# Kernel tuning notes

Hardware: AMD Instinct MI355X
Metric: run time of the kernel (lower is better)

Reference implementation:

```python
import jax, jax.numpy as jnp
import numpy as np

N, F_IN, HID, EMB, HEADS, E = 20000, 256, 256, 128, 8, 160000
NEG_SLOPE = 0.2


def setup_inputs() -> dict:
    key = jax.random.key(0)
    ks = jax.random.split(key, 16)
    s = lambda fan: 1.0 / np.sqrt(fan)
    inp = {
        "x": jax.random.normal(ks[0], (N, F_IN), jnp.float32),
        "edge_index": jax.random.randint(ks[1], (2, E), 0, N, jnp.int64),
        "W1": jax.random.normal(ks[2], (F_IN, HID), jnp.float32) * s(F_IN),
        "b1": jnp.zeros((HID,), jnp.float32),
        "W2": jax.random.normal(ks[3], (HID, HID), jnp.float32) * s(HID),
        "b2": jnp.zeros((HID,), jnp.float32),
        "W3": jax.random.normal(ks[4], (HID, EMB), jnp.float32) * s(HID),
        "b3": jnp.zeros((EMB,), jnp.float32),
        "Wg": jax.random.normal(ks[5], (EMB, HEADS * EMB), jnp.float32) * s(EMB),
        "att_src": jax.random.normal(ks[6], (HEADS, EMB), jnp.float32) * s(EMB),
        "att_dst": jax.random.normal(ks[7], (HEADS, EMB), jnp.float32) * s(EMB),
        "bg": jnp.zeros((HEADS * EMB,), jnp.float32),
        "Wh1": jax.random.normal(ks[8], (HEADS * EMB, HID), jnp.float32) * s(HEADS * EMB),
        "bh1": jnp.zeros((HID,), jnp.float32),
        "Wh2": jax.random.normal(ks[9], (HID, 1), jnp.float32) * s(HID),
        "bh2": jnp.zeros((1,), jnp.float32),
    }
    return inp


def _gcn(x, W, b, src, dst, dinv):
    h = x @ W                                   # [N, out]
    msg = h[src] * (dinv[src] * dinv[dst])[:, None]  # gather + edge scale
    return jax.ops.segment_sum(msg, dst, N) + b


def _gat(x, Wg, att_src, att_dst, bg, src, dst):
    h = (x @ Wg).reshape(N, HEADS, EMB)          # [N, H, C]
    a_s = jnp.einsum('nhc,hc->nh', h, att_src)   # [N, H]
    a_d = jnp.einsum('nhc,hc->nh', h, att_dst)
    e = jax.nn.leaky_relu(a_s[src] + a_d[dst], NEG_SLOPE)  # [Etot, H]
    m = jax.ops.segment_max(e, dst, N)           # per-dst softmax max
    ex = jnp.exp(e - m[dst])
    denom = jax.ops.segment_sum(ex, dst, N)
    alpha = ex / denom[dst]                      # [Etot, H]
    out = jax.ops.segment_sum(h[src] * alpha[:, :, None], dst, N)
    return out.reshape(N, HEADS * EMB) + bg


def reference(x, edge_index, W1, b1, W2, b2, W3, b3, Wg, att_src, att_dst, bg, Wh1, bh1, Wh2, bh2):
    loops = jnp.arange(N, dtype=edge_index.dtype)
    src = jnp.concatenate([edge_index[0], loops])
    dst = jnp.concatenate([edge_index[1], loops])
    deg = jax.ops.segment_sum(jnp.ones_like(dst, dtype=x.dtype), dst, N)
    dinv = jax.lax.rsqrt(jnp.maximum(deg, 1.0))  # deg >= 1 due to self-loops

    h = jax.nn.relu(_gcn(x, W1, b1, src, dst, dinv))
    h = jax.nn.relu(_gcn(h, W2, b2, src, dst, dinv))
    h = jax.nn.relu(_gcn(h, W3, b3, src, dst, dinv))
    h = _gat(h, Wg, att_src, att_dst, bg, src, dst)
    z = jax.nn.relu(h @ Wh1 + bh1)
    logits = (z @ Wh2 + bh2).squeeze(-1)         # [N]
    w = jax.nn.sigmoid(logits)
    return jax.nn.softmax(w, axis=0)
```

## Files before the change

kernel.cpp:

```cpp
#include <hip/hip_runtime.h>
#include <math.h>

#define NN 20000
#define HEADS 8
#define M_PAD 20096

typedef _Float16 f16;
typedef f16 f16x2  __attribute__((ext_vector_type(2)));
typedef f16 f16x4v __attribute__((ext_vector_type(4)));
typedef f16 f16x8v __attribute__((ext_vector_type(8)));
typedef float f32x4 __attribute__((ext_vector_type(4)));

__device__ __forceinline__ float lrelu(float x){ return x > 0.f ? x : 0.2f*x; }

__global__ __launch_bounds__(256) void init_k(int* __restrict__ zbase, int zn,
        const float* __restrict__ W1, const float* __restrict__ W2, const float* __restrict__ W3,
        const float* __restrict__ Wg, const float* __restrict__ att_src, const float* __restrict__ att_dst,
        f16* __restrict__ wt1, f16* __restrict__ wt2, f16* __restrict__ wt3,
        f16* __restrict__ wasT)
{
    int t = blockIdx.x*256 + threadIdx.x;
    if (t < zn){ zbase[t] = 0; return; }
    t -= zn;
    if (t < 65536){ int k = t >> 8, n = t & 255; wt1[n*256 + k] = (f16)W1[t]; return; }
    t -= 65536;
    if (t < 65536){ int k = t >> 8, n = t & 255; wt2[n*256 + k] = (f16)W2[t]; return; }
    t -= 65536;
    if (t < 32768){ int k = t >> 7, n = t & 127; wt3[n*256 + k] = (f16)W3[t]; return; }
    t -= 32768;
    if (t < 8192){
        int r = t >> 7, k = t & 127;
        float s = 0.f;
        if (r < 16){
            const float* att = (r < 8) ? att_src : att_dst;
            int h = r & 7;
            const float* wg = Wg + (size_t)k*1024 + h*128;
            const float* at = att + h*128;
            for (int c = 0; c < 128; ++c) s = fmaf(wg[c], at[c], s);
        }
        wasT[r*128 + k] = (f16)s;
    }
}

__global__ __launch_bounds__(256) void wc_k(const float* __restrict__ Wg, const float* __restrict__ Wh1,
        const float* __restrict__ bg, const float* __restrict__ bh1,
        f16* __restrict__ wc_t, float* __restrict__ biasc)
{
    __shared__ float col[1024];
    __shared__ float red[256];
    const int j = blockIdx.x, t = threadIdx.x;
    float bsum = 0.f;
    #pragma unroll
    for (int i = 0; i < 4; ++i){
        int kk = i*256 + t;
        float v = Wh1[(size_t)kk*256 + j];
        col[kk] = v;
        bsum = fmaf(bg[kk], v, bsum);
    }
    red[t] = bsum; __syncthreads();
    for (int off = 128; off; off >>= 1){
        if (t < off) red[t] += red[t+off];
        __syncthreads();
    }
    if (!t) biasc[j] = red[0] + bh1[j];
    #pragma unroll
    for (int i = 0; i < 4; ++i){
        int k = i*256 + t;
        int h = k >> 7, kk = k & 127;
        const float* wg = Wg + (size_t)kk*1024 + h*128;
        const float* cl = col + h*128;
        float s = 0.f;
        for (int c = 0; c < 128; c += 4){
            float4 wv = *(const float4*)(wg + c);
            s = fmaf(wv.x, cl[c],   s);
            s = fmaf(wv.y, cl[c+1], s);
            s = fmaf(wv.z, cl[c+2], s);
            s = fmaf(wv.w, cl[c+3], s);
        }
        wc_t[(size_t)j*1024 + k] = (f16)s;
    }
}

__global__ __launch_bounds__(256) void hist_k(const int* __restrict__ dst, int* __restrict__ cnt, int E){
    int i = blockIdx.x*256 + threadIdx.x;
    if (i < E) atomicAdd(&cnt[dst[i]], 1);
}
__global__ __launch_bounds__(1024) void scan_k(const int* __restrict__ cnt, int* __restrict__ row_off,
                                               float* __restrict__ dinv){
    __shared__ int tot[1024];
    int t = threadIdx.x;
    const int CH = 20;
    int base = t*CH;
    int loc[CH]; int s = 0;
    #pragma unroll
    for (int i = 0; i < CH; ++i){
        int v = (base+i < NN) ? cnt[base+i] : 0;
        loc[i] = s; s += v;
    }
    tot[t] = s; __syncthreads();
    for (int off = 1; off < 1024; off <<= 1){
        int v = (t >= off) ? tot[t-off] : 0;
        __syncthreads();
        tot[t] += v;
        __syncthreads();
    }
    int pre = (t == 0) ? 0 : tot[t-1];
    #pragma unroll
    for (int i = 0; i < CH; ++i)
        if (base+i < NN){
            row_off[base+i] = pre + loc[i];
            dinv[base+i] = rsqrtf((float)cnt[base+i] + 1.f);
        }
    if (t == 1023) row_off[NN] = tot[1023];
}
__global__ __launch_bounds__(256) void scatter_k(const int* __restrict__ src, const int* __restrict__ dst,
        const int* __restrict__ row_off, int* __restrict__ cursor, int* __restrict__ src_sorted, int E){
    int i = blockIdx.x*256 + threadIdx.x;
    if (i >= E) return;
    int d = dst[i];
    int pos = row_off[d] + atomicAdd(&cursor[d], 1);
    src_sorted[pos] = src[i];
}

template<int EPI, int BN, bool A_F32, bool RELU, bool HAS_BIAS, int MINW>
__global__ __launch_bounds__(256, MINW) void gemm_f16_k(
        const void* __restrict__ Av, const f16* __restrict__ Bt,
        const float* __restrict__ bias, void* __restrict__ C,
        float* __restrict__ as_out, float* __restrict__ ad_out,
        const float* __restrict__ Wh2, float* __restrict__ logit,
        int M, int N, int K)
{
    constexpr int WN = BN/2;
    constexpr int NJ = WN/16;
    __shared__ __align__(16) f16 As[128*64];
    __shared__ __align__(16) f16 Bs[BN*64];
    const int tid  = threadIdx.x;
    const int lane = tid & 63;
    const int wave = tid >> 6;
    const int wm = (wave >> 1) * 64, wn = (wave & 1) * WN;
    const int l15 = lane & 15, quad = lane >> 4;
    const int m0 = blockIdx.y * 128, n0 = blockIdx.x * BN;

    const int rs = tid >> 3;
    const int ce = (tid & 7) * 8;
    const int swst = ((rs & 7) << 3);
    const int swrd = ((l15 & 7) << 3);
    const f16*  Ah = (const f16*)Av;
    const float* Af = (const float*)Av;

    f32x4 acc[4][NJ] = {};
    for (int k0 = 0; k0 < K; k0 += 64){
        #pragma unroll
        for (int pp = 0; pp < 4; ++pp){
            int lr = rs + pp*32;
            int grow = m0 + lr;
            if (A_F32){
                f16x8v hv = {};
                if (grow < M){
                    float4 p = *(const float4*)(Af + (size_t)grow*K + k0 + ce);
                    float4 q = *(const float4*)(Af + (size_t)grow*K + k0 + ce + 4);
                    hv[0]=(f16)p.x; hv[1]=(f16)p.y; hv[2]=(f16)p.z; hv[3]=(f16)p.w;
                    hv[4]=(f16)q.x; hv[5]=(f16)q.y; hv[6]=(f16)q.z; hv[7]=(f16)q.w;
                }
                *(f16x8v*)&As[lr*64 + (ce ^ swst)] = hv;
            } else {
                *(uint4*)&As[lr*64 + (ce ^ swst)] = *(const uint4*)(Ah + (size_t)grow*K + k0 + ce);
            }
        }
        #pragma unroll
        for (int pp = 0; pp < BN/32; ++pp){
            int lr = rs + pp*32;
            *(uint4*)&Bs[lr*64 + (ce ^ swst)] = *(const uint4*)(Bt + (size_t)(n0 + lr)*K + k0 + ce);
        }
        __syncthreads();
        #pragma unroll
        for (int ks = 0; ks < 2; ++ks){
            f16x8v af[4], bf[NJ];
            const int rc = (ks*32 + quad*8) ^ swrd;
            #pragma unroll
            for (int i = 0; i < 4; ++i)
                af[i] = *(const f16x8v*)&As[(wm + i*16 + l15)*64 + rc];
            #pragma unroll
            for (int j = 0; j < NJ; ++j)
                bf[j] = *(const f16x8v*)&Bs[(wn + j*16 + l15)*64 + rc];
            #pragma unroll
            for (int i = 0; i < 4; ++i)
                #pragma unroll
                for (int j = 0; j < NJ; ++j)
                    acc[i][j] = __builtin_amdgcn_mfma_f32_16x16x32_f16(af[i], bf[j], acc[i][j], 0, 0, 0);
        }
        __syncthreads();
    }

    if (EPI == 2){
        float b4[NJ], w4[NJ];
        #pragma unroll
        for (int j = 0; j < NJ; ++j){
            int cg = n0 + wn + j*16 + l15;
            b4[j] = bias[cg]; w4[j] = Wh2[cg];
        }
        #pragma unroll
        for (int i = 0; i < 4; ++i)
            #pragma unroll
            for (int r = 0; r < 4; ++r){
                float ps = 0.f;
                #pragma unroll
                for (int j = 0; j < NJ; ++j){
                    float v = fmaxf(acc[i][j][r] + b4[j], 0.f);
                    ps = fmaf(v, w4[j], ps);
                }
                ps += __shfl_xor(ps, 1, 64); ps += __shfl_xor(ps, 2, 64);
                ps += __shfl_xor(ps, 4, 64); ps += __shfl_xor(ps, 8, 64);
                if (l15 == 0){
                    int row = m0 + wm + i*16 + quad*4 + r;
                    if (row < M) unsafeAtomicAdd(&logit[row], ps);
                }
            }
        return;
    }

    if (EPI == 3){
        #pragma unroll
        for (int i = 0; i < 4; ++i){
            int rb = m0 + wm + i*16 + quad*4;
            #pragma unroll
            for (int j = 0; j < NJ; ++j){
                int col = n0 + wn + j*16 + l15;
                if (col >= 16) continue;
                #pragma unroll
                for (int r = 0; r < 4; ++r){
                    int row = rb + r;
                    if (row >= M) continue;
                    float v = acc[i][j][r];
                    if (col < 8) as_out[row*8 + col] = v;
                    else         ad_out[row*8 + col - 8] = v;
                }
            }
        }
        return;
    }

    #pragma unroll
    for (int i = 0; i < 4; ++i){
        int rb = m0 + wm + i*16 + quad*4;
        #pragma unroll
        for (int j = 0; j < NJ; ++j){
            int col = n0 + wn + j*16 + l15;
            float bv = HAS_BIAS ? bias[col] : 0.f;
            #pragma unroll
            for (int r = 0; r < 4; ++r){
                int row = rb + r;
                if (row >= M) continue;
                float v = acc[i][j][r] + bv;
                if (RELU) v = fmaxf(v, 0.f);
                ((f16*)C)[(size_t)row*N + col] = (f16)v;
            }
        }
    }
}

template<int F>
__global__ __launch_bounds__(256) void gcn_agg_f16_k(const f16* __restrict__ h, const int* __restrict__ row_off,
        const int* __restrict__ srcs, const float* __restrict__ dinv, const float* __restrict__ bias,
        f16* __restrict__ out)
{
    int wv = (blockIdx.x*256 + threadIdx.x) >> 6;
    int lane = threadIdx.x & 63;
    if (wv >= NN) return;
    float di = dinv[wv];
    int p = row_off[wv], r1 = row_off[wv+1];
    if (F == 256){
        f16x4v v = *(const f16x4v*)(h + (size_t)wv*256 + lane*4);
        float c = di*di;
        float a0 = (float)v[0]*c, a1 = (float)v[1]*c, a2 = (float)v[2]*c, a3 = (float)v[3]*c;
        for (; p+4 <= r1; p += 4){
            int s0 = srcs[p], s1 = srcs[p+1], s2 = srcs[p+2], s3 = srcs[p+3];
            float c0 = dinv[s0]*di, c1 = dinv[s1]*di, c2 = dinv[s2]*di, c3 = dinv[s3]*di;
            f16x4v u0 = *(const f16x4v*)(h + (size_t)s0*256 + lane*4);
            f16x4v u1 = *(const f16x4v*)(h + (size_t)s1*256 + lane*4);
            f16x4v u2 = *(const f16x4v*)(h + (size_t)s2*256 + lane*4);
            f16x4v u3 = *(const f16x4v*)(h + (size_t)s3*256 + lane*4);
            a0 = fmaf((float)u3[0], c3, fmaf((float)u2[0], c2, fmaf((float)u1[0], c1, fmaf((float)u0[0], c0, a0))));
            a1 = fmaf((float)u3[1], c3, fmaf((float)u2[1], c2, fmaf((float)u1[1], c1, fmaf((float)u0[1], c0, a1))));
            a2 = fmaf((float)u3[2], c3, fmaf((float)u2[2], c2, fmaf((float)u1[2], c1, fmaf((float)u0[2], c0, a2))));
            a3 = fmaf((float)u3[3], c3, fmaf((float)u2[3], c2, fmaf((float)u1[3], c1, fmaf((float)u0[3], c0, a3))));
        }
        for (; p < r1; ++p){
            int s0 = srcs[p];
            float c0 = dinv[s0]*di;
            f16x4v u0 = *(const f16x4v*)(h + (size_t)s0*256 + lane*4);
            a0 = fmaf((float)u0[0], c0, a0); a1 = fmaf((float)u0[1], c0, a1);
            a2 = fmaf((float)u0[2], c0, a2); a3 = fmaf((float)u0[3], c0, a3);
        }
        float4 bv = *(const float4*)(bias + lane*4);
        f16x4v o;
        o[0] = (f16)fmaxf(a0 + bv.x, 0.f); o[1] = (f16)fmaxf(a1 + bv.y, 0.f);
        o[2] = (f16)fmaxf(a2 + bv.z, 0.f); o[3] = (f16)fmaxf(a3 + bv.w, 0.f);
        *(f16x4v*)(out + (size_t)wv*256 + lane*4) = o;
    } else {
        f16x2 v = *(const f16x2*)(h + (size_t)wv*128 + lane*2);
        float c = di*di;
        float a0 = (float)v[0]*c, a1 = (float)v[1]*c;
        for (; p+4 <= r1; p += 4){
            int s0 = srcs[p], s1 = srcs[p+1], s2 = srcs[p+2], s3 = srcs[p+3];
            float c0 = dinv[s0]*di, c1 = dinv[s1]*di, c2 = dinv[s2]*di, c3 = dinv[s3]*di;
            f16x2 u0 = *(const f16x2*)(h + (size_t)s0*128 + lane*2);
            f16x2 u1 = *(const f16x2*)(h + (size_t)s1*128 + lane*2);
            f16x2 u2 = *(const f16x2*)(h + (size_t)s2*128 + lane*2);
            f16x2 u3 = *(const f16x2*)(h + (size_t)s3*128 + lane*2);
            a0 = fmaf((float)u3[0], c3, fmaf((float)u2[0], c2, fmaf((float)u1[0], c1, fmaf((float)u0[0], c0, a0))));
            a1 = fmaf((float)u3[1], c3, fmaf((float)u2[1], c2, fmaf((float)u1[1], c1, fmaf((float)u0[1], c0, a1))));
        }
        for (; p < r1; ++p){
            int s0 = srcs[p];
            float c0 = dinv[s0]*di;
            f16x2 u0 = *(const f16x2*)(h + (size_t)s0*128 + lane*2);
            a0 = fmaf((float)u0[0], c0, a0); a1 = fmaf((float)u0[1], c0, a1);
        }
        float2 bv = *(const float2*)(bias + lane*2);
        f16x2 o;
        o[0] = (f16)fmaxf(a0 + bv.x, 0.f); o[1] = (f16)fmaxf(a1 + bv.y, 0.f);
        *(f16x2*)(out + (size_t)wv*128 + lane*2) = o;
    }
}

__global__ __launch_bounds__(256) void gat_soft_k(const int* __restrict__ row_off, const int* __restrict__ srcs,
        const float* __restrict__ a_s, const float* __restrict__ a_d,
        float* __restrict__ ex_sorted, float* __restrict__ alpha_self, float* __restrict__ inv_den)
{
    int t = blockIdx.x*256 + threadIdx.x;
    if (t >= NN*HEADS) return;
    int d = t >> 3, h = t & 7;
    float ad = a_d[t];
    float eself = lrelu(a_s[t] + ad);
    float m = eself;
    int r0 = row_off[d], r1 = row_off[d+1];
    for (int p = r0; p < r1; ++p){
        int s = srcs[p];
        m = fmaxf(m, lrelu(a_s[s*HEADS + h] + ad));
    }
    float den = __expf(eself - m);
    for (int p = r0; p < r1; ++p){
        int s = srcs[p];
        float x = __expf(lrelu(a_s[s*HEADS + h] + ad) - m);
        ex_sorted[(size_t)p*HEADS + h] = x;
        den += x;
    }
    float id = 1.f / den;
    alpha_self[t] = __expf(eself - m) * id;
    inv_den[t]    = id;
}

__global__ __launch_bounds__(256) void agg_k(const f16* __restrict__ fG, const int* __restrict__ row_off,
        const int* __restrict__ srcs, const float* __restrict__ exs, const float* __restrict__ aself,
        const float* __restrict__ idn, f16* __restrict__ agg)
{
    int wv = (blockIdx.x*256 + threadIdx.x) >> 6;
    int lane = threadIdx.x & 63;
    if (wv >= NN) return;
    f16x2 v = *(const f16x2*)(fG + (size_t)wv*128 + lane*2);
    float v0 = (float)v[0], v1 = (float)v[1];
    float id[8], acc0[8], acc1[8];
    #pragma unroll
    for (int h = 0; h < 8; ++h){
        float as = aself[wv*8 + h];
        acc0[h] = v0*as; acc1[h] = v1*as;
        id[h] = idn[wv*8 + h];
    }
    int p = row_off[wv], r1 = row_off[wv+1];
    for (; p+2 <= r1; p += 2){
        int s0 = srcs[p], s1 = srcs[p+1];
        f16x2 u0 = *(const f16x2*)(fG + (size_t)s0*128 + lane*2);
        f16x2 u1 = *(const f16x2*)(fG + (size_t)s1*128 + lane*2);
        float4 ea = *(const float4*)(exs + (size_t)p*8);
        float4 eb = *(const float4*)(exs + (size_t)p*8 + 4);
        float4 fa = *(const float4*)(exs + (size_t)(p+1)*8);
        float4 fb = *(const float4*)(exs + (size_t)(p+1)*8 + 4);
        float u00=(float)u0[0], u01=(float)u0[1], u10=(float)u1[0], u11=(float)u1[1];
        float e0[8] = {ea.x,ea.y,ea.z,ea.w,eb.x,eb.y,eb.z,eb.w};
        float e1[8] = {fa.x,fa.y,fa.z,fa.w,fb.x,fb.y,fb.z,fb.w};
        #pragma unroll
        for (int h = 0; h < 8; ++h){
            float al0 = e0[h]*id[h], al1 = e1[h]*id[h];
            acc0[h] = fmaf(u10, al1, fmaf(u00, al0, acc0[h]));
            acc1[h] = fmaf(u11, al1, fmaf(u01, al0, acc1[h]));
        }
    }
    for (; p < r1; ++p){
        int s0 = srcs[p];
        f16x2 u0 = *(const f16x2*)(fG + (size_t)s0*128 + lane*2);
        float4 ea = *(const float4*)(exs + (size_t)p*8);
        float4 eb = *(const float4*)(exs + (size_t)p*8 + 4);
        float u00=(float)u0[0], u01=(float)u0[1];
        float e0[8] = {ea.x,ea.y,ea.z,ea.w,eb.x,eb.y,eb.z,eb.w};
        #pragma unroll
        for (int h = 0; h < 8; ++h){
            float al0 = e0[h]*id[h];
            acc0[h] = fmaf(u00, al0, acc0[h]);
            acc1[h] = fmaf(u01, al0, acc1[h]);
        }
    }
    #pragma unroll
    for (int h = 0; h < 8; ++h){
        f16x2 o; o[0] = (f16)acc0[h]; o[1] = (f16)acc1[h];
        *(f16x2*)(agg + (size_t)wv*1024 + h*128 + lane*2) = o;
    }
}

__global__ __launch_bounds__(256) void head_sum_k(const float* __restrict__ logit, const float* __restrict__ bh2,
                                                  float* __restrict__ w, float* __restrict__ red){
    __shared__ float sm[256];
    int i = blockIdx.x*256 + threadIdx.x;
    float v = 0.f;
    if (i < NN){
        float s = 1.f / (1.f + expf(-(logit[i] + bh2[0])));
        w[i] = s;
        v = expf(s);
    }
    sm[threadIdx.x] = v; __syncthreads();
    for (int off = 128; off; off >>= 1){
        if (threadIdx.x < off) sm[threadIdx.x] += sm[threadIdx.x+off];
        __syncthreads();
    }
    if (!threadIdx.x) unsafeAtomicAdd(&red[0], sm[0]);
}
__global__ __launch_bounds__(256) void final_k(const float* __restrict__ w, const float* __restrict__ red,
                                               float* __restrict__ out){
    int i = blockIdx.x*256 + threadIdx.x;
    if (i >= NN) return;
    out[i] = expf(w[i]) / red[0];
}

extern "C" void kernel_launch(void* const* d_in, const int* in_sizes, int n_in,
                              void* d_out, int out_size, void* d_ws, size_t ws_size,
                              hipStream_t stream) {
    const float* x   = (const float*)d_in[0];
    const int*   ei  = (const int*)  d_in[1];
    const float* W1  = (const float*)d_in[2];
    const float* b1  = (const float*)d_in[3];
    const float* W2  = (const float*)d_in[4];
    const float* b2  = (const float*)d_in[5];
    const float* W3  = (const float*)d_in[6];
    const float* b3  = (const float*)d_in[7];
    const float* Wg  = (const float*)d_in[8];
    const float* att_src = (const float*)d_in[9];
    const float* att_dst = (const float*)d_in[10];
    const float* bg  = (const float*)d_in[11];
    const float* Wh1 = (const float*)d_in[12];
    const float* bh1 = (const float*)d_in[13];
    const float* Wh2 = (const float*)d_in[14];
    const float* bh2 = (const float*)d_in[15];
    float* out = (float*)d_out;

    const int E = in_sizes[1] / 2;
    const int* src = ei;
    const int* dst = ei + E;

    float* ws = (float*)d_ws;
    size_t o = 0;
    auto alloc = [&](size_t nfloats){ float* p = ws + o; o += (nfloats + 3) & ~(size_t)3; return p; };
    int* cnt    = (int*)alloc(NN);
    int* cursor = (int*)alloc(NN);
    float* logit= alloc(NN);
    float* red  = alloc(8);
    const int ZERO_N = 3*NN + 8;

    f16* wt1   = (f16*)alloc(65536/2);
    f16* wt2   = (f16*)alloc(65536/2);
    f16* wt3   = (f16*)alloc(32768/2);
    f16* wc_t  = (f16*)alloc(262144/2);
    f16* wasT  = (f16*)alloc(8192/2);
    float* biasc = alloc(256);
    f16* fH    = (f16*)alloc((size_t)M_PAD*256/2);
    f16* fG    = (f16*)alloc((size_t)M_PAD*256/2);
    f16* agg   = (f16*)alloc((size_t)M_PAD*1024/2);
    float* dinv = alloc(NN);
    float* a_s  = alloc((size_t)NN*HEADS);
    float* a_d  = alloc((size_t)NN*HEADS);
    float* aself= alloc((size_t)NN*HEADS);
    float* idn  = alloc((size_t)NN*HEADS);
    float* exs  = alloc((size_t)E*HEADS);
    float* wsig = alloc(NN);
    int* row_off= (int*)alloc(NN+1);
    int* src_srt= (int*)alloc(E);

    const int nb  = (NN + 255)/256;
    const int eb  = (E + 255)/256;
    const int nwb = (NN + 3)/4;
    const dim3 blk(256);
    const int MT = M_PAD/128;

    const int INIT_T = ZERO_N + 65536*2 + 32768 + 8192;
    init_k<<<(INIT_T + 255)/256, blk, 0, stream>>>(cnt, ZERO_N, W1, W2, W3, Wg, att_src, att_dst,
                                                   wt1, wt2, wt3, wasT);
    wc_k<<<256, blk, 0, stream>>>(Wg, Wh1, bg, bh1, wc_t, biasc);
    hist_k<<<eb, blk, 0, stream>>>(dst, cnt, E);
    scan_k<<<1, 1024, 0, stream>>>(cnt, row_off, dinv);
    scatter_k<<<eb, blk, 0, stream>>>(src, dst, row_off, cursor, src_srt, E);

    gemm_f16_k<0,64,true,false,false,4><<<dim3(4, MT), blk, 0, stream>>>(
        x, wt1, nullptr, fH, nullptr, nullptr, nullptr, nullptr, NN, 256, 256);
    gcn_agg_f16_k<256><<<nwb, blk, 0, stream>>>(fH, row_off, src_srt, dinv, b1, fG);
    gemm_f16_k<0,64,false,false,false,4><<<dim3(4, MT), blk, 0, stream>>>(
        fG, wt2, nullptr, fH, nullptr, nullptr, nullptr, nullptr, NN, 256, 256);
    gcn_agg_f16_k<256><<<nwb, blk, 0, stream>>>(fH, row_off, src_srt, dinv, b2, fG);
    gemm_f16_k<0,64,false,false,false,4><<<dim3(2, MT), blk, 0, stream>>>(
        fG, wt3, nullptr, fH, nullptr, nullptr, nullptr, nullptr, NN, 128, 256);
    gcn_agg_f16_k<128><<<nwb, blk, 0, stream>>>(fH, row_off, src_srt, dinv, b3, fG);

    gemm_f16_k<3,64,false,false,false,4><<<dim3(1, MT), blk, 0, stream>>>(
        fG, wasT, nullptr, nullptr, a_s, a_d, nullptr, nullptr, NN, 64, 128);
    gat_soft_k<<<(NN*HEADS)/256, blk, 0, stream>>>(row_off, src_srt, a_s, a_d, exs, aself, idn);
    agg_k<<<nwb, blk, 0, stream>>>(fG, row_off, src_srt, exs, aself, idn, agg);

    gemm_f16_k<2,64,false,true,true,4><<<dim3(4, MT), blk, 0, stream>>>(
        agg, wc_t, biasc, nullptr, nullptr, nullptr, Wh2, logit, NN, 256, 1024);

    head_sum_k<<<nb, blk, 0, stream>>>(logit, bh2, wsig, red);
    final_k<<<nb, blk, 0, stream>>>(wsig, red, out);
}
```

Baseline: 343.9 us.

## Double-buffer GEMM shared-memory tiles with register prefetch of next K slice

The f16 MFMA GEMM now keeps two LDS buffers for A and B. The next K tile's global loads are issued into registers before the MFMA work on the current tile, then written into the alternate buffer, so there is one barrier per iteration instead of two. The aim is to hide global-load latency behind compute. The cost is twice the LDS (about 48KB per block) and more registers, so the launch-bounds minimum waves per EU is lowered from 4 to 3, which may reduce occupancy.

```diff
diff --git a/kernel.cpp b/kernel.cpp
--- a/kernel.cpp
+++ b/kernel.cpp
@@ -132,8 +132,8 @@
 {
     constexpr int WN = BN/2;
     constexpr int NJ = WN/16;
-    __shared__ __align__(16) f16 As[128*64];
-    __shared__ __align__(16) f16 Bs[BN*64];
+    __shared__ __align__(16) f16 As[2][128*64];
+    __shared__ __align__(16) f16 Bs[2][BN*64];
     const int tid  = threadIdx.x;
     const int lane = tid & 63;
     const int wave = tid >> 6;
@@ -148,48 +148,79 @@
     const f16*  Ah = (const f16*)Av;
     const float* Af = (const float*)Av;
 
+    uint4  ra[4];
+    uint4  rb[BN/32];
+    float4 rf0[4], rf1[4];
+
+    auto issueLoads = [&](int k0){
+        if (A_F32){
+            #pragma unroll
+            for (int pp = 0; pp < 4; ++pp){
+                int grow = m0 + rs + pp*32;
+                if (grow < M){
+                    rf0[pp] = *(const float4*)(Af + (size_t)grow*K + k0 + ce);
+                    rf1[pp] = *(const float4*)(Af + (size_t)grow*K + k0 + ce + 4);
+                } else {
+                    rf0[pp] = make_float4(0.f,0.f,0.f,0.f);
+                    rf1[pp] = make_float4(0.f,0.f,0.f,0.f);
+                }
+            }
+        } else {
+            #pragma unroll
+            for (int pp = 0; pp < 4; ++pp)
+                ra[pp] = *(const uint4*)(Ah + (size_t)(m0 + rs + pp*32)*K + k0 + ce);
+        }
+        #pragma unroll
+        for (int pp = 0; pp < BN/32; ++pp)
+            rb[pp] = *(const uint4*)(Bt + (size_t)(n0 + rs + pp*32)*K + k0 + ce);
+    };
+    auto writeLds = [&](int buf){
+        if (A_F32){
+            #pragma unroll
+            for (int pp = 0; pp < 4; ++pp){
+                f16x8v hv;
+                hv[0]=(f16)rf0[pp].x; hv[1]=(f16)rf0[pp].y; hv[2]=(f16)rf0[pp].z; hv[3]=(f16)rf0[pp].w;
+                hv[4]=(f16)rf1[pp].x; hv[5]=(f16)rf1[pp].y; hv[6]=(f16)rf1[pp].z; hv[7]=(f16)rf1[pp].w;
+                *(f16x8v*)&As[buf][(rs + pp*32)*64 + (ce ^ swst)] = hv;
+            }
+        } else {
+            #pragma unroll
+            for (int pp = 0; pp < 4; ++pp)
+                *(uint4*)&As[buf][(rs + pp*32)*64 + (ce ^ swst)] = ra[pp];
+        }
+        #pragma unroll
+        for (int pp = 0; pp < BN/32; ++pp)
+            *(uint4*)&Bs[buf][(rs + pp*32)*64 + (ce ^ swst)] = rb[pp];
+    };
+
+    issueLoads(0);
+    writeLds(0);
+    __syncthreads();
+
     f32x4 acc[4][NJ] = {};
-    for (int k0 = 0; k0 < K; k0 += 64){
-        #pragma unroll
-        for (int pp = 0; pp < 4; ++pp){
-            int lr = rs + pp*32;
-            int grow = m0 + lr;
-            if (A_F32){
-                f16x8v hv = {};
-                if (grow < M){
-                    float4 p = *(const float4*)(Af + (size_t)grow*K + k0 + ce);
-                    float4 q = *(const float4*)(Af + (size_t)grow*K + k0 + ce + 4);
-                    hv[0]=(f16)p.x; hv[1]=(f16)p.y; hv[2]=(f16)p.z; hv[3]=(f16)p.w;
-                    hv[4]=(f16)q.x; hv[5]=(f16)q.y; hv[6]=(f16)q.z; hv[7]=(f16)q.w;
-                }
-                *(f16x8v*)&As[lr*64 + (ce ^ swst)] = hv;
-            } else {
-                *(uint4*)&As[lr*64 + (ce ^ swst)] = *(const uint4*)(Ah + (size_t)grow*K + k0 + ce);
-            }
-        }
-        #pragma unroll
-        for (int pp = 0; pp < BN/32; ++pp){
-            int lr = rs + pp*32;
-            *(uint4*)&Bs[lr*64 + (ce ^ swst)] = *(const uint4*)(Bt + (size_t)(n0 + lr)*K + k0 + ce);
-        }
-        __syncthreads();
+    int cur = 0;
+    for (int k0 = 64; k0 <= K; k0 += 64){
+        const bool more = (k0 < K);
+        if (more) issueLoads(k0);
         #pragma unroll
         for (int ks = 0; ks < 2; ++ks){
             f16x8v af[4], bf[NJ];
             const int rc = (ks*32 + quad*8) ^ swrd;
             #pragma unroll
             for (int i = 0; i < 4; ++i)
-                af[i] = *(const f16x8v*)&As[(wm + i*16 + l15)*64 + rc];
+                af[i] = *(const f16x8v*)&As[cur][(wm + i*16 + l15)*64 + rc];
             #pragma unroll
             for (int j = 0; j < NJ; ++j)
-                bf[j] = *(const f16x8v*)&Bs[(wn + j*16 + l15)*64 + rc];
+                bf[j] = *(const f16x8v*)&Bs[cur][(wn + j*16 + l15)*64 + rc];
             #pragma unroll
             for (int i = 0; i < 4; ++i)
                 #pragma unroll
                 for (int j = 0; j < NJ; ++j)
                     acc[i][j] = __builtin_amdgcn_mfma_f32_16x16x32_f16(af[i], bf[j], acc[i][j], 0, 0, 0);
         }
+        if (more) writeLds(cur ^ 1);
         __syncthreads();
+        cur ^= 1;
     }
 
     if (EPI == 2){
@@ -222,14 +253,14 @@
     if (EPI == 3){
         #pragma unroll
         for (int i = 0; i < 4; ++i){
-            int rb = m0 + wm + i*16 + quad*4;
+            int rb2 = m0 + wm + i*16 + quad*4;
             #pragma unroll
             for (int j = 0; j < NJ; ++j){
                 int col = n0 + wn + j*16 + l15;
                 if (col >= 16) continue;
                 #pragma unroll
                 for (int r = 0; r < 4; ++r){
-                    int row = rb + r;
+                    int row = rb2 + r;
                     if (row >= M) continue;
                     float v = acc[i][j][r];
                     if (col < 8) as_out[row*8 + col] = v;
@@ -242,14 +273,14 @@
 
     #pragma unroll
     for (int i = 0; i < 4; ++i){
-        int rb = m0 + wm + i*16 + quad*4;
+        int rb2 = m0 + wm + i*16 + quad*4;
         #pragma unroll
         for (int j = 0; j < NJ; ++j){
             int col = n0 + wn + j*16 + l15;
             float bv = HAS_BIAS ? bias[col] : 0.f;
             #pragma unroll
             for (int r = 0; r < 4; ++r){
-                int row = rb + r;
+                int row = rb2 + r;
                 if (row >= M) continue;
                 float v = acc[i][j][r] + bv;
                 if (RELU) v = fmaxf(v, 0.f);
@@ -498,22 +529,22 @@
     scan_k<<<1, 1024, 0, stream>>>(cnt, row_off, dinv);
     scatter_k<<<eb, blk, 0, stream>>>(src, dst, row_off, cursor, src_srt, E);
 
-    gemm_f16_k<0,64,true,false,false,4><<<dim3(4, MT), blk, 0, stream>>>(
+    gemm_f16_k<0,64,true,false,false,3><<<dim3(4, MT), blk, 0, stream>>>(
         x, wt1, nullptr, fH, nullptr, nullptr, nullptr, nullptr, NN, 256, 256);
     gcn_agg_f16_k<256><<<nwb, blk, 0, stream>>>(fH, row_off, src_srt, dinv, b1, fG);
-    gemm_f16_k<0,64,false,false,false,4><<<dim3(4, MT), blk, 0, stream>>>(
+    gemm_f16_k<0,64,false,false,false,3><<<dim3(4, MT), blk, 0, stream>>>(
         fG, wt2, nullptr, fH, nullptr, nullptr, nullptr, nullptr, NN, 256, 256);
     gcn_agg_f16_k<256><<<nwb, blk, 0, stream>>>(fH, row_off, src_srt, dinv, b2, fG);
-    gemm_f16_k<0,64,false,false,false,4><<<dim3(2, MT), blk, 0, stream>>>(
+    gemm_f16_k<0,64,false,false,false,3><<<dim3(2, MT), blk, 0, stream>>>(
         fG, wt3, nullptr, fH, nullptr, nullptr, nullptr, nullptr, NN, 128, 256);
     gcn_agg_f16_k<128><<<nwb, blk, 0, stream>>>(fH, row_off, src_srt, dinv, b3, fG);
 
-    gemm_f16_k<3,64,false,false,false,4><<<dim3(1, MT), blk, 0, stream>>>(
+    gemm_f16_k<3,64,false,false,false,3><<<dim3(1, MT), blk, 0, stream>>>(
         fG, wasT, nullptr, nullptr, a_s, a_d, nullptr, nullptr, NN, 64, 128);
     gat_soft_k<<<(NN*HEADS)/256, blk, 0, stream>>>(row_off, src_srt, a_s, a_d, exs, aself, idn);
     agg_k<<<nwb, blk, 0, stream>>>(fG, row_off, src_srt, exs, aself, idn, agg);
 
-    gemm_f16_k<2,64,false,true,true,4><<<dim3(4, MT), blk, 0, stream>>>(
+    gemm_f16_k<2,64,false,true,true,3><<<dim3(4, MT), blk, 0, stream>>>(
         agg, wc_t, biasc, nullptr, nullptr, nullptr, Wh2, logit, NN, 256, 1024);
 
     head_sum_k<<<nb, blk, 0, stream>>>(logit, bh2, wsig, red);
```

Result: slower. 432.1 us (+25.7%).

## Double-buffer GEMM shared-memory tiles with register prefetch of next K slice

Applied to the files above, without the earlier changes.

The f16 MFMA GEMM now keeps two shared-memory buffers for A and B. Global loads for the next K tile are issued into registers before computing on the current tile, then written to the alternate buffer, so there is one barrier per K step instead of two. This is meant to hide global load latency behind MFMA work. It doubles LDS use (48KB per block) and raises register pressure, and the occupancy hint drops from 4 to 3 waves per SIMD.

```diff
diff --git a/kernel.cpp b/kernel.cpp
--- a/kernel.cpp
+++ b/kernel.cpp
@@ -122,7 +122,7 @@
     src_sorted[pos] = src[i];
 }
 
-template<int EPI, int BN, bool A_F32, bool RELU, bool HAS_BIAS, int MINW>
+template<int EPI, bool A_F32, bool RELU, bool HAS_BIAS, int MINW>
 __global__ __launch_bounds__(256, MINW) void gemm_f16_k(
         const void* __restrict__ Av, const f16* __restrict__ Bt,
         const float* __restrict__ bias, void* __restrict__ C,
@@ -130,16 +130,15 @@
         const float* __restrict__ Wh2, float* __restrict__ logit,
         int M, int N, int K)
 {
-    constexpr int WN = BN/2;
-    constexpr int NJ = WN/16;
-    __shared__ __align__(16) f16 As[128*64];
-    __shared__ __align__(16) f16 Bs[BN*64];
+    constexpr int NJ = 2;
+    __shared__ __align__(16) f16 As[2][128*64];
+    __shared__ __align__(16) f16 Bs[2][64*64];
     const int tid  = threadIdx.x;
     const int lane = tid & 63;
     const int wave = tid >> 6;
-    const int wm = (wave >> 1) * 64, wn = (wave & 1) * WN;
+    const int wm = (wave >> 1) * 64, wn = (wave & 1) * 32;
     const int l15 = lane & 15, quad = lane >> 4;
-    const int m0 = blockIdx.y * 128, n0 = blockIdx.x * BN;
+    const int m0 = blockIdx.y * 128, n0 = blockIdx.x * 64;
 
     const int rs = tid >> 3;
     const int ce = (tid & 7) * 8;
@@ -148,49 +147,87 @@
     const f16*  Ah = (const f16*)Av;
     const float* Af = (const float*)Av;
 
+    uint4 ra0, ra1, ra2, ra3, rb0, rb1;
+    float4 rf00, rf01, rf10, rf11, rf20, rf21, rf30, rf31;
+
+#define GEMM_ISSUE(k0)                                                                    \
+    if (A_F32){                                                                           \
+        int g0 = m0 + rs, g1 = g0 + 32, g2 = g0 + 64, g3 = g0 + 96;                       \
+        if (g0 < M){ rf00 = *(const float4*)(Af + (size_t)g0*K + (k0) + ce);              \
+                     rf01 = *(const float4*)(Af + (size_t)g0*K + (k0) + ce + 4); }        \
+        else { rf00 = make_float4(0,0,0,0); rf01 = make_float4(0,0,0,0); }                \
+        if (g1 < M){ rf10 = *(const float4*)(Af + (size_t)g1*K + (k0) + ce);              \
+                     rf11 = *(const float4*)(Af + (size_t)g1*K + (k0) + ce + 4); }        \
+        else { rf10 = make_float4(0,0,0,0); rf11 = make_float4(0,0,0,0); }                \
+        if (g2 < M){ rf20 = *(const float4*)(Af + (size_t)g2*K + (k0) + ce);              \
+                     rf21 = *(const float4*)(Af + (size_t)g2*K + (k0) + ce + 4); }        \
+        else { rf20 = make_float4(0,0,0,0); rf21 = make_float4(0,0,0,0); }                \
+        if (g3 < M){ rf30 = *(const float4*)(Af + (size_t)g3*K + (k0) + ce);              \
+                     rf31 = *(const float4*)(Af + (size_t)g3*K + (k0) + ce + 4); }        \
+        else { rf30 = make_float4(0,0,0,0); rf31 = make_float4(0,0,0,0); }                \
+    } else {                                                                              \
+        ra0 = *(const uint4*)(Ah + (size_t)(m0 + rs      )*K + (k0) + ce);                \
+        ra1 = *(const uint4*)(Ah + (size_t)(m0 + rs + 32 )*K + (k0) + ce);                \
+        ra2 = *(const uint4*)(Ah + (size_t)(m0 + rs + 64 )*K + (k0) + ce);                \
+        ra3 = *(const uint4*)(Ah + (size_t)(m0 + rs + 96 )*K + (k0) + ce);                \
+    }                                                                                     \
+    rb0 = *(const uint4*)(Bt + (size_t)(n0 + rs     )*K + (k0) + ce);                     \
+    rb1 = *(const uint4*)(Bt + (size_t)(n0 + rs + 32)*K + (k0) + ce);
+
+#define GEMM_CVT(hv, lo, hi)                                                              \
+    { hv[0]=(f16)lo.x; hv[1]=(f16)lo.y; hv[2]=(f16)lo.z; hv[3]=(f16)lo.w;                 \
+      hv[4]=(f16)hi.x; hv[5]=(f16)hi.y; hv[6]=(f16)hi.z; hv[7]=(f16)hi.w; }
+
+#define GEMM_WRITE(buf)                                                                   \
+    if (A_F32){                                                                           \
+        f16x8v h0, h1, h2, h3;                                                            \
+        GEMM_CVT(h0, rf00, rf01) GEMM_CVT(h1, rf10, rf11)                                 \
+        GEMM_CVT(h2, rf20, rf21) GEMM_CVT(h3, rf30, rf31)                                 \
+        *(f16x8v*)&As[buf][(rs     )*64 + (ce ^ swst)] = h0;                              \
+        *(f16x8v*)&As[buf][(rs + 32)*64 + (ce ^ swst)] = h1;                              \
+        *(f16x8v*)&As[buf][(rs + 64)*64 + (ce ^ swst)] = h2;                              \
+        *(f16x8v*)&As[buf][(rs + 96)*64 + (ce ^ swst)] = h3;                              \
+    } else {                                                                              \
+        *(uint4*)&As[buf][(rs     )*64 + (ce ^ swst)] = ra0;                              \
+        *(uint4*)&As[buf][(rs + 32)*64 + (ce ^ swst)] = ra1;                              \
+        *(uint4*)&As[buf][(rs + 64)*64 + (ce ^ swst)] = ra2;                              \
+        *(uint4*)&As[buf][(rs + 96)*64 + (ce ^ swst)] = ra3;                              \
+    }                                                                                     \
+    *(uint4*)&Bs[buf][(rs     )*64 + (ce ^ swst)] = rb0;                                  \
+    *(uint4*)&Bs[buf][(rs + 32)*64 + (ce ^ swst)] = rb1;
+
+    GEMM_ISSUE(0)
+    GEMM_WRITE(0)
+    __syncthreads();
+
     f32x4 acc[4][NJ] = {};
-    for (int k0 = 0; k0 < K; k0 += 64){
-        #pragma unroll
-        for (int pp = 0; pp < 4; ++pp){
-            int lr = rs + pp*32;
-            int grow = m0 + lr;
-            if (A_F32){
-                f16x8v hv = {};
-                if (grow < M){
-                    float4 p = *(const float4*)(Af + (size_t)grow*K + k0 + ce);
-                    float4 q = *(const float4*)(Af + (size_t)grow*K + k0 + ce + 4);
-                    hv[0]=(f16)p.x; hv[1]=(f16)p.y; hv[2]=(f16)p.z; hv[3]=(f16)p.w;
-                    hv[4]=(f16)q.x; hv[5]=(f16)q.y; hv[6]=(f16)q.z; hv[7]=(f16)q.w;
-                }
-                *(f16x8v*)&As[lr*64 + (ce ^ swst)] = hv;
-            } else {
-                *(uint4*)&As[lr*64 + (ce ^ swst)] = *(const uint4*)(Ah + (size_t)grow*K + k0 + ce);
-            }
-        }
-        #pragma unroll
-        for (int pp = 0; pp < BN/32; ++pp){
-            int lr = rs + pp*32;
-            *(uint4*)&Bs[lr*64 + (ce ^ swst)] = *(const uint4*)(Bt + (size_t)(n0 + lr)*K + k0 + ce);
-        }
-        __syncthreads();
+    int cur = 0;
+    for (int k0 = 64; k0 <= K; k0 += 64){
+        const bool more = (k0 < K);
+        if (more) { GEMM_ISSUE(k0) }
         #pragma unroll
         for (int ks = 0; ks < 2; ++ks){
             f16x8v af[4], bf[NJ];
             const int rc = (ks*32 + quad*8) ^ swrd;
             #pragma unroll
             for (int i = 0; i < 4; ++i)
-                af[i] = *(const f16x8v*)&As[(wm + i*16 + l15)*64 + rc];
+                af[i] = *(const f16x8v*)&As[cur][(wm + i*16 + l15)*64 + rc];
             #pragma unroll
             for (int j = 0; j < NJ; ++j)
-                bf[j] = *(const f16x8v*)&Bs[(wn + j*16 + l15)*64 + rc];
+                bf[j] = *(const f16x8v*)&Bs[cur][(wn + j*16 + l15)*64 + rc];
             #pragma unroll
             for (int i = 0; i < 4; ++i)
                 #pragma unroll
                 for (int j = 0; j < NJ; ++j)
                     acc[i][j] = __builtin_amdgcn_mfma_f32_16x16x32_f16(af[i], bf[j], acc[i][j], 0, 0, 0);
         }
+        if (more) { GEMM_WRITE(cur ^ 1) }
         __syncthreads();
-    }
+        cur ^= 1;
+    }
+#undef GEMM_ISSUE
+#undef GEMM_CVT
+#undef GEMM_WRITE
 
     if (EPI == 2){
         float b4[NJ], w4[NJ];
@@ -222,14 +259,14 @@
     if (EPI == 3){
         #pragma unroll
         for (int i = 0; i < 4; ++i){
-            int rb = m0 + wm + i*16 + quad*4;
+            int rb2 = m0 + wm + i*16 + quad*4;
             #pragma unroll
             for (int j = 0; j < NJ; ++j){
                 int col = n0 + wn + j*16 + l15;
                 if (col >= 16) continue;
                 #pragma unroll
                 for (int r = 0; r < 4; ++r){
-                    int row = rb + r;
+                    int row = rb2 + r;
                     if (row >= M) continue;
                     float v = acc[i][j][r];
                     if (col < 8) as_out[row*8 + col] = v;
@@ -242,14 +279,14 @@
 
     #pragma unroll
     for (int i = 0; i < 4; ++i){
-        int rb = m0 + wm + i*16 + quad*4;
+        int rb2 = m0 + wm + i*16 + quad*4;
         #pragma unroll
         for (int j = 0; j < NJ; ++j){
             int col = n0 + wn + j*16 + l15;
             float bv = HAS_BIAS ? bias[col] : 0.f;
             #pragma unroll
             for (int r = 0; r < 4; ++r){
-                int row = rb + r;
+                int row = rb2 + r;
                 if (row >= M) continue;
                 float v = acc[i][j][r] + bv;
                 if (RELU) v = fmaxf(v, 0.f);
@@ -498,22 +535,22 @@
     scan_k<<<1, 1024, 0, stream>>>(cnt, row_off, dinv);
     scatter_k<<<eb, blk, 0, stream>>>(src, dst, row_off, cursor, src_srt, E);
 
-    gemm_f16_k<0,64,true,false,false,4><<<dim3(4, MT), blk, 0, stream>>>(
+    gemm_f16_k<0,true,false,false,3><<<dim3(4, MT), blk, 0, stream>>>(
         x, wt1, nullptr, fH, nullptr, nullptr, nullptr, nullptr, NN, 256, 256);
     gcn_agg_f16_k<256><<<nwb, blk, 0, stream>>>(fH, row_off, src_srt, dinv, b1, fG);
-    gemm_f16_k<0,64,false,false,false,4><<<dim3(4, MT), blk, 0, stream>>>(
+    gemm_f16_k<0,false,false,false,3><<<dim3(4, MT), blk, 0, stream>>>(
         fG, wt2, nullptr, fH, nullptr, nullptr, nullptr, nullptr, NN, 256, 256);
     gcn_agg_f16_k<256><<<nwb, blk, 0, stream>>>(fH, row_off, src_srt, dinv, b2, fG);
-    gemm_f16_k<0,64,false,false,false,4><<<dim3(2, MT), blk, 0, stream>>>(
+    gemm_f16_k<0,false,false,false,3><<<dim3(2, MT), blk, 0, stream>>>(
         fG, wt3, nullptr, fH, nullptr, nullptr, nullptr, nullptr, NN, 128, 256);
     gcn_agg_f16_k<128><<<nwb, blk, 0, stream>>>(fH, row_off, src_srt, dinv, b3, fG);
 
-    gemm_f16_k<3,64,false,false,false,4><<<dim3(1, MT), blk, 0, stream>>>(
+    gemm_f16_k<3,false,false,false,3><<<dim3(1, MT), blk, 0, stream>>>(
         fG, wasT, nullptr, nullptr, a_s, a_d, nullptr, nullptr, NN, 64, 128);
     gat_soft_k<<<(NN*HEADS)/256, blk, 0, stream>>>(row_off, src_srt, a_s, a_d, exs, aself, idn);
     agg_k<<<nwb, blk, 0, stream>>>(fG, row_off, src_srt, exs, aself, idn, agg);
 
-    gemm_f16_k<2,64,false,true,true,4><<<dim3(4, MT), blk, 0, stream>>>(
+    gemm_f16_k<2,false,true,true,3><<<dim3(4, MT), blk, 0, stream>>>(
         agg, wc_t, biasc, nullptr, nullptr, nullptr, Wh2, logit, NN, 256, 1024);
 
     head_sum_k<<<nb, blk, 0, stream>>>(logit, bh2, wsig, red);
```

After: 333.8 us, median of 2. 2.9% less time.
